# Kernel tuning notes

Hardware: AMD Instinct MI355X
Metric: run time of the kernel (lower is better)

Reference implementation:

```python
import jax, jax.numpy as jnp
import numpy as np

D_MODEL = 1024
NUM_HEADS = 16
D_K = D_MODEL // NUM_HEADS
B, S = 2, 2048


def setup_inputs() -> dict:
    key = jax.random.key(0)
    ks = jax.random.split(key, 10)
    scale = 1.0 / np.sqrt(D_MODEL)
    inp = {
        "x": jax.random.normal(ks[0], (B, S, D_MODEL), dtype=jnp.float32),
        "mask": jax.random.randint(ks[1], (B, S, S), 0, 2, dtype=jnp.int32),
        "Wq": jax.random.normal(ks[2], (D_MODEL, D_MODEL), dtype=jnp.float32) * scale,
        "bq": jnp.zeros((D_MODEL,), dtype=jnp.float32),
        "Wk": jax.random.normal(ks[3], (D_MODEL, D_MODEL), dtype=jnp.float32) * scale,
        "bk": jnp.zeros((D_MODEL,), dtype=jnp.float32),
        "Wv": jax.random.normal(ks[4], (D_MODEL, D_MODEL), dtype=jnp.float32) * scale,
        "bv": jnp.zeros((D_MODEL,), dtype=jnp.float32),
        "Wo": jax.random.normal(ks[5], (D_MODEL, D_MODEL), dtype=jnp.float32) * scale,
        "bo": jnp.zeros((D_MODEL,), dtype=jnp.float32),
    }
    return inp


def reference(x, mask, Wq, bq, Wk, bk, Wv, bv, Wo, bo):
    # x: [B,S,D]; Linear is x @ W.T + b (torch convention: W is [out,in])
    b, s, _ = x.shape
    def proj(W, bias):
        h = jnp.einsum('bsd,ed->bse', x, W) + bias          # [B,S,D]
        return h.reshape(b, s, NUM_HEADS, D_K).transpose(0, 2, 1, 3)  # [B,H,S,Dk]
    Q = proj(Wq, bq)
    K = proj(Wk, bk)
    V = proj(Wv, bv)
    scores = jnp.einsum('bhqd,bhkd->bhqk', Q, K) / np.sqrt(D_K)  # [B,H,S,S]
    # mask==0 positions get -1e9 (mask broadcast over heads)
    scores = jnp.where(mask[:, None, :, :] == 0, jnp.float32(-1e9), scores)
    attn = jax.nn.softmax(scores, axis=-1)
    # dropout is identity in eval/deterministic mode
    out = jnp.einsum('bhqk,bhkd->bhqd', attn, V)  # [B,H,S,Dk]
    out = out.transpose(0, 2, 1, 3).reshape(b, s, D_MODEL)
    return jnp.einsum('bsd,ed->bse', out, Wo) + bo
```

## Files before the change

kernel.cpp:

```cpp
#include <hip/hip_runtime.h>


#define B_DIM 2
#define S_DIM 2048
#define H_DIM 16
#define DK 64
#define DM 1024
#define MROWS (B_DIM * S_DIM)

typedef __attribute__((ext_vector_type(8))) short bf16x8;
typedef __attribute__((ext_vector_type(4))) float f32x4;
typedef __attribute__((ext_vector_type(16))) float f32x16;

__device__ __forceinline__ unsigned short f2bf(float f) {
  union { float f; unsigned u; } v; v.f = f;
  unsigned r = v.u + 0x7fffu + ((v.u >> 16) & 1u);
  return (unsigned short)(r >> 16);
}

__device__ __forceinline__ unsigned cvtpk(float lo, float hi_) {
  unsigned r;
  asm("v_cvt_pk_bf16_f32 %0, %1, %2" : "=v"(r) : "v"(lo), "v"(hi_));
  return r;
}

__device__ __forceinline__ float fexp2(float x) {
  float r;
  asm("v_exp_f32 %0, %1" : "=v"(r) : "v"(x));
  return r;
}

__device__ __forceinline__ void async_ld16(unsigned short* lds, const unsigned short* g) {
  __builtin_amdgcn_global_load_lds(
      (const __attribute__((address_space(1))) unsigned int*)g,
      (__attribute__((address_space(3))) unsigned int*)lds,
      16, 0, 0);
}

__global__ __launch_bounds__(256) void conv_kernel(const float* __restrict__ src,
                                                   unsigned short* __restrict__ dst,
                                                   int n4) {
  int i = blockIdx.x * 256 + threadIdx.x;
  if (i < n4) {
    float4 v = ((const float4*)src)[i];
    ushort4 o;
    o.x = f2bf(v.x); o.y = f2bf(v.y); o.z = f2bf(v.z); o.w = f2bf(v.w);
    ((ushort4*)dst)[i] = o;
  }
}

__global__ __launch_bounds__(256) void maskpack_kernel(const int* __restrict__ mask,
                                                       unsigned* __restrict__ mp,
                                                       int nw) {
  int t = blockIdx.x * 256 + threadIdx.x;
  if (t >= nw) return;
  const int4* p = (const int4*)mask + (size_t)t * 8;
  unsigned w = 0;
#pragma unroll
  for (int j = 0; j < 8; ++j) {
    int4 v = p[j];
    w |= (v.x != 0 ? 1u : 0u) << (j * 4 + 0);
    w |= (v.y != 0 ? 1u : 0u) << (j * 4 + 1);
    w |= (v.z != 0 ? 1u : 0u) << (j * 4 + 2);
    w |= (v.w != 0 ? 1u : 0u) << (j * 4 + 3);
  }
  mp[t] = w;
}

template <int MODE>
__global__ __launch_bounds__(256) void gemm_bt_kernel(
    const unsigned short* __restrict__ A, const unsigned short* __restrict__ B,
    const int M, const int N, const int K,
    unsigned short* __restrict__ Qo, unsigned short* __restrict__ Ko,
    unsigned short* __restrict__ Vo,
    const float* __restrict__ bq, const float* __restrict__ bk,
    const float* __restrict__ bv,
    float* __restrict__ fout, const float* __restrict__ fbias) {
  __shared__ unsigned short sA[128 * 32];
  __shared__ unsigned short sB[128 * 32];
  const int t = threadIdx.x;
  const int l = t & 63;
  const int w = t >> 6;
  const int q = l & 15, g = l >> 4;
  const int wr = w >> 1, wc = w & 1;
  const int nbn = N >> 7;
  const int mb = blockIdx.x / nbn;
  const int nb = blockIdx.x % nbn;

  const f32x4 fzero = {0.f, 0.f, 0.f, 0.f};
  f32x4 acc[4][4];
#pragma unroll
  for (int i = 0; i < 4; ++i)
#pragma unroll
    for (int j = 0; j < 4; ++j) acc[i][j] = fzero;

  const int steps = K >> 5;
  for (int kb = 0; kb < steps; ++kb) {
#pragma unroll
    for (int i = 0; i < 2; ++i) {
      const int idx = i * 256 + t;
      const int row = idx >> 2;
      const int c8 = (idx & 3) * 8;
      async_ld16(&sA[idx * 8], A + (mb * 128 + row) * K + kb * 32 + c8);
      async_ld16(&sB[idx * 8], B + (nb * 128 + row) * K + kb * 32 + c8);
    }
    __syncthreads();
    bf16x8 af[4], bfr[4];
#pragma unroll
    for (int mi = 0; mi < 4; ++mi)
      af[mi] = *(const bf16x8*)&sA[(wr * 64 + mi * 16 + q) * 32 + g * 8];
#pragma unroll
    for (int nj = 0; nj < 4; ++nj)
      bfr[nj] = *(const bf16x8*)&sB[(wc * 64 + nj * 16 + q) * 32 + g * 8];
#pragma unroll
    for (int mi = 0; mi < 4; ++mi)
#pragma unroll
      for (int nj = 0; nj < 4; ++nj)
        acc[mi][nj] = __builtin_amdgcn_mfma_f32_16x16x32_bf16(af[mi], bfr[nj],
                                                              acc[mi][nj], 0, 0, 0);
    __syncthreads();
  }

#pragma unroll
  for (int mi = 0; mi < 4; ++mi) {
    const int mbase = mb * 128 + wr * 64 + mi * 16 + g * 4;
#pragma unroll
    for (int nj = 0; nj < 4; ++nj) {
      const int n = nb * 128 + wc * 64 + nj * 16 + q;
      f32x4 c = acc[mi][nj];
      if (MODE == 0) {
        const int which = n >> 10;
        const int e = n & 1023;
        const int h = e >> 6, dk = e & 63;
        const float bias = (which == 0 ? bq : which == 1 ? bk : bv)[e];
        if (which == 2) {
          const int bi = mbase >> 11, s = mbase & 2047;
          const int bh2 = bi * H_DIM + h;
          ushort4 v4;
          v4.x = f2bf(c[0] + bias);
          v4.y = f2bf(c[1] + bias);
          v4.z = f2bf(c[2] + bias);
          v4.w = f2bf(c[3] + bias);
          *(ushort4*)&Vo[((size_t)bh2 * DK + dk) * S_DIM + s] = v4;
        } else {
          unsigned short* dst = (which == 0) ? Qo : Ko;
#pragma unroll
          for (int r = 0; r < 4; ++r) {
            const int m = mbase + r;
            const int bi = m >> 11, s = m & 2047;
            dst[((size_t)(bi * H_DIM + h) * S_DIM + s) * DK + dk] = f2bf(c[r] + bias);
          }
        }
      } else {
        const float bias = fbias[n];
#pragma unroll
        for (int r = 0; r < 4; ++r) {
          const int m = mbase + r;
          fout[(size_t)m * N + n] = c[r] + bias;
        }
      }
    }
  }
}

__global__ __launch_bounds__(256) void attn_kernel(
    const unsigned short* __restrict__ Qb, const unsigned short* __restrict__ Kb,
    const unsigned short* __restrict__ Vtb, const unsigned* __restrict__ mp,
    unsigned short* __restrict__ Ob) {
  const int t = threadIdx.x, l = t & 63, w = t >> 6;
  const int gw = blockIdx.x * 4 + w;
  const int bh = gw >> 6;
  const int qt = gw & 63;
  const int qbase = qt * 32;
  const int b = bh >> 4, h = bh & 15;
  const int q = l & 31, hi = l >> 5;

  const unsigned short* Qh = Qb + (size_t)bh * S_DIM * DK;
  const unsigned short* Kh = Kb + (size_t)bh * S_DIM * DK;
  const unsigned short* Vh = Vtb + (size_t)bh * DK * S_DIM;
  const unsigned* mrow = mp + ((size_t)b * S_DIM + qbase + q) * (S_DIM / 32);

  bf16x8 qf[4];
#pragma unroll
  for (int ds = 0; ds < 4; ++ds)
    qf[ds] = *(const bf16x8*)(Qh + (qbase + q) * DK + ds * 16 + hi * 8);

  const float NEG = -3.0e38f;
  float m_run = NEG;
  float l_run = 0.f;
  f32x16 accT0 = {0.f,0.f,0.f,0.f,0.f,0.f,0.f,0.f,0.f,0.f,0.f,0.f,0.f,0.f,0.f,0.f};
  f32x16 accT1 = accT0;
  const f32x16 zero16 = accT0;
  const float SC2 = 0.125f * 1.4426950408889634f;

  bf16x8 nk[4], nv[2][2];
#pragma unroll
  for (int ds = 0; ds < 4; ++ds)
    nk[ds] = *(const bf16x8*)(Kh + (0 + q) * DK + ds * 16 + hi * 8);
#pragma unroll
  for (int dt = 0; dt < 2; ++dt)
#pragma unroll
    for (int st = 0; st < 2; ++st)
      nv[dt][st] = *(const bf16x8*)(Vh + (dt * 32 + q) * S_DIM + 0 + st * 16 + hi * 8);
  unsigned nmw = mrow[0];

  for (int kt = 0; kt < 64; ++kt) {
    const bf16x8 ck0 = nk[0], ck1 = nk[1], ck2 = nk[2], ck3 = nk[3];
    const bf16x8 cv00 = nv[0][0], cv01 = nv[0][1], cv10 = nv[1][0], cv11 = nv[1][1];
    const unsigned cmw = nmw;
    {
      const int ktn = (kt < 63) ? kt + 1 : 0;
      const int kn = ktn * 32;
#pragma unroll
      for (int ds = 0; ds < 4; ++ds)
        nk[ds] = *(const bf16x8*)(Kh + (kn + q) * DK + ds * 16 + hi * 8);
#pragma unroll
      for (int dt = 0; dt < 2; ++dt)
#pragma unroll
        for (int st = 0; st < 2; ++st)
          nv[dt][st] = *(const bf16x8*)(Vh + (dt * 32 + q) * S_DIM + kn + st * 16 + hi * 8);
      nmw = mrow[ktn];
    }

    f32x16 T = zero16;
    T = __builtin_amdgcn_mfma_f32_32x32x16_bf16(ck0, qf[0], T, 0, 0, 0);
    T = __builtin_amdgcn_mfma_f32_32x32x16_bf16(ck1, qf[1], T, 0, 0, 0);
    T = __builtin_amdgcn_mfma_f32_32x32x16_bf16(ck2, qf[2], T, 0, 0, 0);
    T = __builtin_amdgcn_mfma_f32_32x32x16_bf16(ck3, qf[3], T, 0, 0, 0);

    const unsigned mws = cmw >> (4 * hi);
    float s[16];
#pragma unroll
    for (int r = 0; r < 16; ++r) {
      const int c = (r & 3) + 8 * (r >> 2);
      s[r] = ((mws >> c) & 1u) ? T[r] * SC2 : NEG;
    }
    float tm = s[0];
#pragma unroll
    for (int r = 1; r < 16; ++r) tm = fmaxf(tm, s[r]);
    tm = fmaxf(tm, __shfl_xor(tm, 32, 64));

    if (__any(tm > m_run)) {
      const float m_new = fmaxf(m_run, tm);
      const float fs = fexp2(m_run - m_new);
#pragma unroll
      for (int r = 0; r < 16; ++r) { accT0[r] *= fs; accT1[r] *= fs; }
      l_run *= fs;
      m_run = m_new;
    }

    float p[16];
    float ts = 0.f;
#pragma unroll
    for (int r = 0; r < 16; ++r) {
      p[r] = fexp2(s[r] - m_run);
      ts += p[r];
    }
    ts += __shfl_xor(ts, 32, 64);
    l_run += ts;

    unsigned pw[8];
#pragma unroll
    for (int st = 0; st < 2; ++st) {
      const int r0 = st * 8;
      const unsigned a0 = cvtpk(p[r0 + 0], p[r0 + 1]);
      const unsigned a1 = cvtpk(p[r0 + 2], p[r0 + 3]);
      const unsigned a2 = cvtpk(p[r0 + 4], p[r0 + 5]);
      const unsigned a3 = cvtpk(p[r0 + 6], p[r0 + 7]);
      const unsigned a0x = (unsigned)__shfl_xor((int)a0, 32, 64);
      const unsigned a1x = (unsigned)__shfl_xor((int)a1, 32, 64);
      const unsigned a2x = (unsigned)__shfl_xor((int)a2, 32, 64);
      const unsigned a3x = (unsigned)__shfl_xor((int)a3, 32, 64);
      pw[st * 4 + 0] = hi ? a2x : a0;
      pw[st * 4 + 1] = hi ? a3x : a1;
      pw[st * 4 + 2] = hi ? a2 : a0x;
      pw[st * 4 + 3] = hi ? a3 : a1x;
    }
    union { unsigned u[4]; bf16x8 v; } pf0, pf1;
    pf0.u[0] = pw[0]; pf0.u[1] = pw[1]; pf0.u[2] = pw[2]; pf0.u[3] = pw[3];
    pf1.u[0] = pw[4]; pf1.u[1] = pw[5]; pf1.u[2] = pw[6]; pf1.u[3] = pw[7];

    accT0 = __builtin_amdgcn_mfma_f32_32x32x16_bf16(cv00, pf0.v, accT0, 0, 0, 0);
    accT0 = __builtin_amdgcn_mfma_f32_32x32x16_bf16(cv01, pf1.v, accT0, 0, 0, 0);
    accT1 = __builtin_amdgcn_mfma_f32_32x32x16_bf16(cv10, pf0.v, accT1, 0, 0, 0);
    accT1 = __builtin_amdgcn_mfma_f32_32x32x16_bf16(cv11, pf1.v, accT1, 0, 0, 0);
  }

  const float linv = 1.0f / l_run;
  unsigned short* orow = Ob + ((size_t)b * S_DIM + qbase + q) * DM + h * DK;
#pragma unroll
  for (int dt = 0; dt < 2; ++dt) {
#pragma unroll
    for (int rp = 0; rp < 8; ++rp) {
      const int r = rp * 2;
      const int d0 = (r & 3) + 8 * (r >> 2) + 4 * hi;
      const float v0 = (dt ? accT1[r] : accT0[r]) * linv;
      const float v1 = (dt ? accT1[r + 1] : accT0[r + 1]) * linv;
      *(unsigned*)&orow[dt * 32 + d0] = cvtpk(v0, v1);
    }
  }
}

extern "C" void kernel_launch(void* const* d_in, const int* in_sizes, int n_in,
                              void* d_out, int out_size, void* d_ws, size_t ws_size,
                              hipStream_t stream) {
  (void)in_sizes; (void)n_in; (void)out_size; (void)ws_size;
  const float* x  = (const float*)d_in[0];
  const int* mask = (const int*)d_in[1];
  const float* Wq = (const float*)d_in[2];
  const float* bq = (const float*)d_in[3];
  const float* Wk = (const float*)d_in[4];
  const float* bk = (const float*)d_in[5];
  const float* Wv = (const float*)d_in[6];
  const float* bv = (const float*)d_in[7];
  const float* Wo = (const float*)d_in[8];
  const float* bo = (const float*)d_in[9];
  float* out = (float*)d_out;

  char* ws = (char*)d_ws;
  unsigned short* Xb   = (unsigned short*)(ws + 0);
  unsigned short* Wqkv = (unsigned short*)(ws + (8u << 20));
  unsigned short* Wob  = (unsigned short*)(ws + 14680064);
  unsigned short* Qbuf = (unsigned short*)(ws + 16777216);
  unsigned short* Kbuf = (unsigned short*)(ws + 25165824);
  unsigned short* Vtb  = (unsigned short*)(ws + 33554432);
  unsigned short* Obuf = (unsigned short*)(ws + 41943040);
  unsigned* Mp         = (unsigned*)(ws + 50331648);

  conv_kernel<<<4096, 256, 0, stream>>>(x, Xb, 1048576);
  conv_kernel<<<1024, 256, 0, stream>>>(Wq, Wqkv + 0 * 1048576, 262144);
  conv_kernel<<<1024, 256, 0, stream>>>(Wk, Wqkv + 1 * 1048576, 262144);
  conv_kernel<<<1024, 256, 0, stream>>>(Wv, Wqkv + 2 * 1048576, 262144);
  conv_kernel<<<1024, 256, 0, stream>>>(Wo, Wob, 262144);
  maskpack_kernel<<<1024, 256, 0, stream>>>(mask, Mp, 262144);
  gemm_bt_kernel<0><<<32 * 24, 256, 0, stream>>>(Xb, Wqkv, MROWS, 3 * DM, DM,
                                                 Qbuf, Kbuf, Vtb, bq, bk, bv,
                                                 nullptr, nullptr);
  attn_kernel<<<512, 256, 0, stream>>>(Qbuf, Kbuf, Vtb, Mp, Obuf);
  gemm_bt_kernel<1><<<32 * 8, 256, 0, stream>>>(Obuf, Wob, MROWS, DM, DM,
                                                nullptr, nullptr, nullptr,
                                                nullptr, nullptr, nullptr,
                                                out, bo);
}
```

Baseline: 319.1 us.

## Share K/V/mask tiles across waves via double-buffered async LDS loads

The attention kernel previously had each wave prefetch its own K, V and mask tiles from global memory into registers. Now the four waves of a block handle consecutive query tiles of the same head and share one K/V/mask tile in LDS. That tile is filled with async global-to-LDS loads into a double buffer, using an XOR swizzle to avoid bank conflicts. This cuts redundant global/L2 traffic for K and V by the number of waves per block. In exchange it adds a block-wide barrier every key tile and depends on the async LDS loads completing before that barrier.

```diff
diff --git a/kernel.cpp b/kernel.cpp
--- a/kernel.cpp
+++ b/kernel.cpp
@@ -35,6 +35,13 @@
       (const __attribute__((address_space(1))) unsigned int*)g,
       (__attribute__((address_space(3))) unsigned int*)lds,
       16, 0, 0);
+}
+
+__device__ __forceinline__ void async_ld4(unsigned* lds, const unsigned* g) {
+  __builtin_amdgcn_global_load_lds(
+      (const __attribute__((address_space(1))) unsigned int*)g,
+      (__attribute__((address_space(3))) unsigned int*)lds,
+      4, 0, 0);
 }
 
 __global__ __launch_bounds__(256) void conv_kernel(const float* __restrict__ src,
@@ -167,18 +174,27 @@
     const unsigned short* __restrict__ Qb, const unsigned short* __restrict__ Kb,
     const unsigned short* __restrict__ Vtb, const unsigned* __restrict__ mp,
     unsigned short* __restrict__ Ob) {
+  __shared__ unsigned short sK[2][2048];
+  __shared__ unsigned short sV[2][2048];
+  __shared__ unsigned smask[2][128];
+
   const int t = threadIdx.x, l = t & 63, w = t >> 6;
-  const int gw = blockIdx.x * 4 + w;
-  const int bh = gw >> 6;
-  const int qt = gw & 63;
-  const int qbase = qt * 32;
+  const int bh = blockIdx.x >> 4;
+  const int qb = blockIdx.x & 15;
+  const int qbase = qb * 128 + w * 32;
   const int b = bh >> 4, h = bh & 15;
   const int q = l & 31, hi = l >> 5;
 
   const unsigned short* Qh = Qb + (size_t)bh * S_DIM * DK;
   const unsigned short* Kh = Kb + (size_t)bh * S_DIM * DK;
   const unsigned short* Vh = Vtb + (size_t)bh * DK * S_DIM;
-  const unsigned* mrow = mp + ((size_t)b * S_DIM + qbase + q) * (S_DIM / 32);
+
+  const int rS = t >> 3;
+  const int cgS = (t & 7) ^ (rS & 7);
+  const unsigned short* gK = Kh + rS * DK + cgS * 8;
+  const int dV = rS + 32 * (cgS >> 2);
+  const unsigned short* gV = Vh + (size_t)dV * S_DIM + (cgS & 3) * 8;
+  const unsigned* gm = mp + ((size_t)b * S_DIM + qb * 128 + w * 64 + l) * (S_DIM / 32);
 
   bf16x8 qf[4];
 #pragma unroll
@@ -192,41 +208,39 @@
   f32x16 accT1 = accT0;
   const f32x16 zero16 = accT0;
   const float SC2 = 0.125f * 1.4426950408889634f;
-
-  bf16x8 nk[4], nv[2][2];
-#pragma unroll
-  for (int ds = 0; ds < 4; ++ds)
-    nk[ds] = *(const bf16x8*)(Kh + (0 + q) * DK + ds * 16 + hi * 8);
-#pragma unroll
-  for (int dt = 0; dt < 2; ++dt)
-#pragma unroll
-    for (int st = 0; st < 2; ++st)
-      nv[dt][st] = *(const bf16x8*)(Vh + (dt * 32 + q) * S_DIM + 0 + st * 16 + hi * 8);
-  unsigned nmw = mrow[0];
+  const int swz = q & 7;
+
+  async_ld16(&sK[0][t * 8], gK);
+  async_ld16(&sV[0][t * 8], gV);
+  if (w < 2) async_ld4(&smask[0][w * 64 + l], gm);
+  __syncthreads();
 
   for (int kt = 0; kt < 64; ++kt) {
-    const bf16x8 ck0 = nk[0], ck1 = nk[1], ck2 = nk[2], ck3 = nk[3];
-    const bf16x8 cv00 = nv[0][0], cv01 = nv[0][1], cv10 = nv[1][0], cv11 = nv[1][1];
-    const unsigned cmw = nmw;
-    {
-      const int ktn = (kt < 63) ? kt + 1 : 0;
-      const int kn = ktn * 32;
-#pragma unroll
-      for (int ds = 0; ds < 4; ++ds)
-        nk[ds] = *(const bf16x8*)(Kh + (kn + q) * DK + ds * 16 + hi * 8);
-#pragma unroll
-      for (int dt = 0; dt < 2; ++dt)
-#pragma unroll
-        for (int st = 0; st < 2; ++st)
-          nv[dt][st] = *(const bf16x8*)(Vh + (dt * 32 + q) * S_DIM + kn + st * 16 + hi * 8);
-      nmw = mrow[ktn];
-    }
+    const int cur = kt & 1;
+    if (kt < 63) {
+      const int ktn = kt + 1;
+      async_ld16(&sK[cur ^ 1][t * 8], gK + ktn * 2048);
+      async_ld16(&sV[cur ^ 1][t * 8], gV + ktn * 32);
+      if (w < 2) async_ld4(&smask[cur ^ 1][w * 64 + l], gm + ktn);
+    }
+
+    bf16x8 ck[4];
+#pragma unroll
+    for (int ds = 0; ds < 4; ++ds)
+      ck[ds] = *(const bf16x8*)&sK[cur][q * 64 + (((ds * 2 + hi) ^ swz) * 8)];
+    bf16x8 cv[2][2];
+#pragma unroll
+    for (int dt = 0; dt < 2; ++dt)
+#pragma unroll
+      for (int st = 0; st < 2; ++st)
+        cv[dt][st] = *(const bf16x8*)&sV[cur][q * 64 + (((dt * 4 + st * 2 + hi) ^ swz) * 8)];
+    const unsigned cmw = smask[cur][w * 32 + q];
 
     f32x16 T = zero16;
-    T = __builtin_amdgcn_mfma_f32_32x32x16_bf16(ck0, qf[0], T, 0, 0, 0);
-    T = __builtin_amdgcn_mfma_f32_32x32x16_bf16(ck1, qf[1], T, 0, 0, 0);
-    T = __builtin_amdgcn_mfma_f32_32x32x16_bf16(ck2, qf[2], T, 0, 0, 0);
-    T = __builtin_amdgcn_mfma_f32_32x32x16_bf16(ck3, qf[3], T, 0, 0, 0);
+    T = __builtin_amdgcn_mfma_f32_32x32x16_bf16(ck[0], qf[0], T, 0, 0, 0);
+    T = __builtin_amdgcn_mfma_f32_32x32x16_bf16(ck[1], qf[1], T, 0, 0, 0);
+    T = __builtin_amdgcn_mfma_f32_32x32x16_bf16(ck[2], qf[2], T, 0, 0, 0);
+    T = __builtin_amdgcn_mfma_f32_32x32x16_bf16(ck[3], qf[3], T, 0, 0, 0);
 
     const unsigned mws = cmw >> (4 * hi);
     float s[16];
@@ -280,10 +294,12 @@
     pf0.u[0] = pw[0]; pf0.u[1] = pw[1]; pf0.u[2] = pw[2]; pf0.u[3] = pw[3];
     pf1.u[0] = pw[4]; pf1.u[1] = pw[5]; pf1.u[2] = pw[6]; pf1.u[3] = pw[7];
 
-    accT0 = __builtin_amdgcn_mfma_f32_32x32x16_bf16(cv00, pf0.v, accT0, 0, 0, 0);
-    accT0 = __builtin_amdgcn_mfma_f32_32x32x16_bf16(cv01, pf1.v, accT0, 0, 0, 0);
-    accT1 = __builtin_amdgcn_mfma_f32_32x32x16_bf16(cv10, pf0.v, accT1, 0, 0, 0);
-    accT1 = __builtin_amdgcn_mfma_f32_32x32x16_bf16(cv11, pf1.v, accT1, 0, 0, 0);
+    accT0 = __builtin_amdgcn_mfma_f32_32x32x16_bf16(cv[0][0], pf0.v, accT0, 0, 0, 0);
+    accT0 = __builtin_amdgcn_mfma_f32_32x32x16_bf16(cv[0][1], pf1.v, accT0, 0, 0, 0);
+    accT1 = __builtin_amdgcn_mfma_f32_32x32x16_bf16(cv[1][0], pf0.v, accT1, 0, 0, 0);
+    accT1 = __builtin_amdgcn_mfma_f32_32x32x16_bf16(cv[1][1], pf1.v, accT1, 0, 0, 0);
+
+    __syncthreads();
   }
 
   const float linv = 1.0f / l_run;
```

Measured after the change: 274.0 us. 14.1% less time.
